# Performance work log

Measured on AMD Instinct MI355X. Metric: run time of the kernel, lower is better.

Reference implementation:

```python
import jax, jax.numpy as jnp
import numpy as np

DIM = 1024
QK_DIM = 128
HIDDEN = 2048  # int(2.0 * DIM)
B, N = 4, 4096


def setup_inputs() -> dict:
    key = jax.random.key(0)
    ks = jax.random.split(key, 10)
    std = 0.02
    return {
        "x": jax.random.normal(ks[0], (B, N, DIM), dtype=jnp.float32),
        "ln_g": jnp.ones((DIM,), jnp.float32),
        "ln_b": jnp.zeros((DIM,), jnp.float32),
        "W_hidden": jax.random.normal(ks[1], (DIM, 2 * HIDDEN), jnp.float32) * (1.0 / np.sqrt(DIM)),
        "b_hidden": jnp.zeros((2 * HIDDEN,), jnp.float32),
        "W_qk": jax.random.normal(ks[2], (DIM, QK_DIM), jnp.float32) * (1.0 / np.sqrt(DIM)),
        "b_qk": jnp.zeros((QK_DIM,), jnp.float32),
        "os_gamma": jax.random.normal(ks[3], (2, QK_DIM), jnp.float32) * std,
        "os_beta": jnp.zeros((2, QK_DIM), jnp.float32),
        "W_out": jax.random.normal(ks[4], (HIDDEN, DIM), jnp.float32) * (1.0 / np.sqrt(HIDDEN)),
        "b_out": jnp.zeros((DIM,), jnp.float32),
    }


def _layernorm(x, g, b, eps=1e-5):
    mu = jnp.mean(x, axis=-1, keepdims=True)
    var = jnp.var(x, axis=-1, keepdims=True)
    return (x - mu) * jax.lax.rsqrt(var + eps) * g + b


def reference(x, ln_g, ln_b, W_hidden, b_hidden, W_qk, b_qk, os_gamma, os_beta, W_out, b_out):
    n = x.shape[-2]
    normed = _layernorm(x, ln_g, ln_b)
    hidden = jax.nn.silu(normed @ W_hidden + b_hidden)  # [b,n,2*hidden]
    v, gate = jnp.split(hidden, 2, axis=-1)             # [b,n,hidden] each
    qk = jax.nn.silu(normed @ W_qk + b_qk)              # [b,n,qk]
    q = qk * os_gamma[0] + os_beta[0]
    k = qk * os_gamma[1] + os_beta[1]
    sim = jnp.einsum('bid,bjd->bij', q, k)
    # causal: divide row i by (i+1)
    denom = (jnp.arange(n, dtype=x.dtype) + 1.0)[:, None]  # [n,1]
    sim = sim / denom
    attn = jnp.square(jax.nn.relu(sim))
    causal_mask = jnp.triu(jnp.ones((n, n), dtype=bool), k=1)
    attn = jnp.where(causal_mask, 0.0, attn)
    out = jnp.einsum('bij,bjd->bid', attn, v)
    out = out * gate
    out = out @ W_out + b_out
    return out + x
```

## Files before the change

kernel.cpp:

```cpp
#include <hip/hip_runtime.h>
#include <hip/hip_bf16.h>
#include <stdint.h>

typedef __bf16 bf16_t;
typedef __bf16 bf16x4 __attribute__((ext_vector_type(4)));
typedef __bf16 bf16x8 __attribute__((ext_vector_type(8)));
typedef float  f32x4  __attribute__((ext_vector_type(4)));

#define MFMA16(a, b, c) __builtin_amdgcn_mfma_f32_16x16x32_bf16((a), (b), (c), 0, 0, 0)

static constexpr int TOKS   = 16384;
static constexpr int SEQ    = 4096;
static constexpr int DIMK   = 1024;
static constexpr int H2     = 4096;
static constexpr int HID    = 2048;
static constexpr int QKD    = 128;
static constexpr int SMEM8P = 131072;
static constexpr size_t PBATCH = 8912896;

__device__ __forceinline__ void gload_lds16(const bf16_t* g, bf16_t* l) {
  __builtin_amdgcn_global_load_lds((__attribute__((address_space(1))) void*)(g),
                                   (__attribute__((address_space(3))) void*)(l),
                                   16, 0, 0);
}

__device__ __forceinline__ float silu_f(float v) { return v / (1.0f + __expf(-v)); }

#define BARRIER() do { __builtin_amdgcn_sched_barrier(0); \
                       __builtin_amdgcn_s_barrier();      \
                       __builtin_amdgcn_sched_barrier(0); } while (0)

__global__ __launch_bounds__(256) void k_transpose_bf16(const float* __restrict__ W,
                                                        bf16_t* __restrict__ WT,
                                                        int K, int N) {
  __shared__ float t[32][33];
  int n0 = blockIdx.x * 32, k0 = blockIdx.y * 32;
  int tx = threadIdx.x & 31, ty = threadIdx.x >> 5;
#pragma unroll
  for (int r = 0; r < 32; r += 8)
    t[ty + r][tx] = W[(size_t)(k0 + ty + r) * N + n0 + tx];
  __syncthreads();
#pragma unroll
  for (int r = 0; r < 32; r += 8)
    WT[(size_t)(n0 + ty + r) * K + k0 + tx] = (bf16_t)t[tx][ty + r];
}

__global__ __launch_bounds__(256) void k_layernorm(const float* __restrict__ x,
                                                   const float* __restrict__ g,
                                                   const float* __restrict__ b,
                                                   bf16_t* __restrict__ out) {
  int row = blockIdx.x, t = threadIdx.x;
  const float4* xr = (const float4*)(x + (size_t)row * DIMK);
  float4 v = xr[t];
  float s  = v.x + v.y + v.z + v.w;
  float ss = v.x * v.x + v.y * v.y + v.z * v.z + v.w * v.w;
#pragma unroll
  for (int o = 1; o < 64; o <<= 1) { s += __shfl_xor(s, o); ss += __shfl_xor(ss, o); }
  __shared__ float red[8];
  int wave = t >> 6, lane = t & 63;
  if (lane == 0) { red[wave] = s; red[wave + 4] = ss; }
  __syncthreads();
  s  = red[0] + red[1] + red[2] + red[3];
  ss = red[4] + red[5] + red[6] + red[7];
  float mean = s * (1.0f / DIMK);
  float var  = ss * (1.0f / DIMK) - mean * mean;
  float rstd = rsqrtf(var + 1e-5f);
  float4 gg = ((const float4*)g)[t];
  float4 bb = ((const float4*)b)[t];
  bf16x4 o4;
  o4[0] = (bf16_t)((v.x - mean) * rstd * gg.x + bb.x);
  o4[1] = (bf16_t)((v.y - mean) * rstd * gg.y + bb.y);
  o4[2] = (bf16_t)((v.z - mean) * rstd * gg.z + bb.z);
  o4[3] = (bf16_t)((v.w - mean) * rstd * gg.w + bb.w);
  *(bf16x4*)(out + (size_t)row * DIMK + t * 4) = o4;
}

#define MFMAQ(MH, KK)                                                         \
  _Pragma("unroll")                                                           \
  for (int mi = 0; mi < 4; ++mi)                                              \
    _Pragma("unroll")                                                         \
    for (int nj = 0; nj < 4; ++nj)                                            \
      acc[(MH) * 4 + mi][nj] =                                                \
          MFMA16(aF[(MH) * 4 + mi][KK], bF[nj][KK], acc[(MH) * 4 + mi][nj]);

__device__ __forceinline__ void core8p(const bf16_t* __restrict__ Ag, int lda,
                                       const bf16_t* __restrict__ Bg, int ldb,
                                       int NK, bf16_t* AS, bf16_t* BS,
                                       f32x4 (&acc)[8][4]) {
  const int tid = threadIdx.x, wid = tid >> 6, lane = tid & 63;
  const int wm = wid >> 2, wn = wid & 3;
  const int srow = lane >> 3;
  const int scol = ((lane & 7) ^ srow) * 8;

  auto stA = [&](int kt, int h) {
    const bf16_t* s = Ag + (size_t)(h * 128 + wid * 16 + srow) * lda + kt * 64 + scol;
    bf16_t* d = AS + ((kt & 1) * 2 + h) * 8192 + wid * 1024;
    gload_lds16(s, d);
    gload_lds16(s + 8 * lda, d + 512);
  };
  auto stB = [&](int kt, int h) {
    const bf16_t* s = Bg + (size_t)(h * 128 + wid * 16 + srow) * ldb + kt * 64 + scol;
    bf16_t* d = BS + ((kt & 1) * 2 + h) * 8192 + wid * 1024;
    gload_lds16(s, d);
    gload_lds16(s + 8 * ldb, d + 512);
  };

  const int g0 = (lane >> 4) ^ (lane & 7);
  const bf16_t* pA0 = AS + wm * 8192 + (lane & 15) * 64 + g0 * 8;
  const bf16_t* pA1 = AS + wm * 8192 + (lane & 15) * 64 + (g0 ^ 4) * 8;
  const bf16_t* pB0 = BS + (wn >> 1) * 8192 + ((wn & 1) * 64 + (lane & 15)) * 64 + g0 * 8;
  const bf16_t* pB1 = BS + (wn >> 1) * 8192 + ((wn & 1) * 64 + (lane & 15)) * 64 + (g0 ^ 4) * 8;

  bf16x8 aF[8][2], bF[4][2];

  stA(0, 0); stA(0, 1); stB(0, 0); stB(0, 1);
  stA(1, 0); stA(1, 1);
  asm volatile("s_waitcnt vmcnt(4)" ::: "memory");
  BARRIER();

  for (int g = 0; g < NK; ++g) {
    const int buf = (g & 1) * 16384;
#pragma unroll
    for (int mi = 0; mi < 8; ++mi) aF[mi][0] = *(const bf16x8*)(pA0 + buf + mi * 1024);
#pragma unroll
    for (int nj = 0; nj < 4; ++nj) bF[nj][0] = *(const bf16x8*)(pB0 + buf + nj * 1024);
    if (g + 1 < NK) stB(g + 1, 0);
    BARRIER();
    __builtin_amdgcn_s_setprio(1);
    MFMAQ(0, 0);
    __builtin_amdgcn_s_setprio(0);
    BARRIER();
#pragma unroll
    for (int mi = 0; mi < 8; ++mi) aF[mi][1] = *(const bf16x8*)(pA1 + buf + mi * 1024);
    if (g + 1 < NK) stB(g + 1, 1);
    BARRIER();
    __builtin_amdgcn_s_setprio(1);
    MFMAQ(1, 0);
    __builtin_amdgcn_s_setprio(0);
    BARRIER();
#pragma unroll
    for (int nj = 0; nj < 4; ++nj) bF[nj][1] = *(const bf16x8*)(pB1 + buf + nj * 1024);
    if (g + 2 < NK) stA(g + 2, 0);
    BARRIER();
    __builtin_amdgcn_s_setprio(1);
    MFMAQ(0, 1);
    __builtin_amdgcn_s_setprio(0);
    BARRIER();
    if (g + 2 < NK) stA(g + 2, 1);
    BARRIER();
    __builtin_amdgcn_s_setprio(1);
    MFMAQ(1, 1);
    __builtin_amdgcn_s_setprio(0);
    if (g < NK - 2)       { asm volatile("s_waitcnt vmcnt(4)" ::: "memory"); }
    else if (g == NK - 2) { asm volatile("s_waitcnt vmcnt(0)" ::: "memory"); }
    BARRIER();
  }
}

__global__ __launch_bounds__(512, 2) void k_gemm_hidden8p(const bf16_t* __restrict__ A,
                                                          const bf16_t* __restrict__ BT,
                                                          const float* __restrict__ bias,
                                                          bf16_t* __restrict__ vT,
                                                          bf16_t* __restrict__ gate) {
  extern __shared__ __align__(16) char lds[];
  bf16_t* AS = (bf16_t*)lds;
  bf16_t* BS = AS + 32768;
  const int nwg = gridDim.x, bid = blockIdx.x;
  const int swz = (bid & 7) * (nwg >> 3) + (bid >> 3);
  const int mblk = swz >> 4, nblk = swz & 15;
  const int m0 = mblk * 256, n0 = nblk * 256;
  f32x4 acc[8][4];
#pragma unroll
  for (int i = 0; i < 8; ++i)
#pragma unroll
    for (int j = 0; j < 4; ++j) acc[i][j] = (f32x4){0.f, 0.f, 0.f, 0.f};
  core8p(A + (size_t)m0 * DIMK, DIMK, BT + (size_t)n0 * DIMK, DIMK,
         DIMK / 64, AS, BS, acc);

  const int tid = threadIdx.x, wid = tid >> 6, lane = tid & 63;
  const int wm = wid >> 2, wn = wid & 3;
  const int row0 = m0 + wm * 128, col0 = n0 + wn * 64;
#pragma unroll
  for (int mi = 0; mi < 8; ++mi)
#pragma unroll
    for (int nj = 0; nj < 4; ++nj) {
      int col = col0 + nj * 16 + (lane & 15);
      float bv = bias[col];
      int row = row0 + mi * 16 + ((lane >> 4) << 2);
      float sv[4];
#pragma unroll
      for (int r = 0; r < 4; ++r) sv[r] = silu_f(acc[mi][nj][r] + bv);
      if (col < HID) {
        bf16x4 pk;
#pragma unroll
        for (int r = 0; r < 4; ++r) pk[r] = (bf16_t)sv[r];
        *(bf16x4*)(vT + (size_t)col * TOKS + row) = pk;
      } else {
#pragma unroll
        for (int r = 0; r < 4; ++r)
          gate[(size_t)(row + r) * HID + (col - HID)] = (bf16_t)sv[r];
      }
    }
}

__global__ __launch_bounds__(512, 2) void k_gemm_out8p(const bf16_t* __restrict__ A,
                                                       const bf16_t* __restrict__ BT,
                                                       const float* __restrict__ bo,
                                                       const float* __restrict__ x,
                                                       float* __restrict__ out) {
  extern __shared__ __align__(16) char lds[];
  bf16_t* AS = (bf16_t*)lds;
  bf16_t* BS = AS + 32768;
  const int nwg = gridDim.x, bid = blockIdx.x;
  const int swz = (bid & 7) * (nwg >> 3) + (bid >> 3);
  const int mblk = swz >> 2, nblk = swz & 3;
  const int m0 = mblk * 256, n0 = nblk * 256;
  f32x4 acc[8][4];
#pragma unroll
  for (int i = 0; i < 8; ++i)
#pragma unroll
    for (int j = 0; j < 4; ++j) acc[i][j] = (f32x4){0.f, 0.f, 0.f, 0.f};
  core8p(A + (size_t)m0 * HID, HID, BT + (size_t)n0 * HID, HID,
         HID / 64, AS, BS, acc);

  const int tid = threadIdx.x, wid = tid >> 6, lane = tid & 63;
  const int wm = wid >> 2, wn = wid & 3;
  const int row0 = m0 + wm * 128, col0 = n0 + wn * 64;
#pragma unroll
  for (int mi = 0; mi < 8; ++mi)
#pragma unroll
    for (int nj = 0; nj < 4; ++nj) {
      int col = col0 + nj * 16 + (lane & 15);
      float bv = bo[col];
      int row = row0 + mi * 16 + ((lane >> 4) << 2);
#pragma unroll
      for (int r = 0; r < 4; ++r) {
        size_t gi = (size_t)(row + r) * DIMK + col;
        out[gi] = acc[mi][nj][r] + bv + x[gi];
      }
    }
}

__global__ __launch_bounds__(512, 2) void k_pv8p(const bf16_t* __restrict__ Pb,
                                                 const bf16_t* __restrict__ vT,
                                                 bf16_t* __restrict__ gate) {
  extern __shared__ __align__(16) char lds[];
  bf16_t* AS = (bf16_t*)lds;
  bf16_t* BS = AS + 32768;
  const int w = blockIdx.x;
  const int rb = 15 - (w >> 5);
  const int hb = (w >> 2) & 7;
  const int bb = w & 3;
  const int lda = (rb + 1) * 256;
  const bf16_t* Ag = Pb + (size_t)bb * PBATCH + (size_t)65536 * (rb * (rb + 1) / 2);
  const bf16_t* Bg = vT + (size_t)(hb * 256) * TOKS + (size_t)bb * SEQ;
  f32x4 acc[8][4];
#pragma unroll
  for (int i = 0; i < 8; ++i)
#pragma unroll
    for (int j = 0; j < 4; ++j) acc[i][j] = (f32x4){0.f, 0.f, 0.f, 0.f};
  core8p(Ag, lda, Bg, TOKS, (rb + 1) * 4, AS, BS, acc);

  const int tid = threadIdx.x, wid = tid >> 6, lane = tid & 63;
  const int wm = wid >> 2, wn = wid & 3;
  const int row0 = rb * 256 + wm * 128, col0 = hb * 256 + wn * 64;
#pragma unroll
  for (int mi = 0; mi < 8; ++mi)
#pragma unroll
    for (int nj = 0; nj < 4; ++nj) {
      int col = col0 + nj * 16 + (lane & 15);
      int row = row0 + mi * 16 + ((lane >> 4) << 2);
#pragma unroll
      for (int r = 0; r < 4; ++r) {
        size_t gi = (size_t)(bb * SEQ + row + r) * HID + col;
        float gv = (float)gate[gi];
        gate[gi] = (bf16_t)(acc[mi][nj][r] * gv);
      }
    }
}

__device__ __forceinline__ void gemm_core_std(const bf16_t* __restrict__ Ag0, int lda,
                                              const bf16_t* __restrict__ Bg0, int ldb,
                                              int K, bf16_t* As, bf16_t* Bs,
                                              f32x4 acc[4][4]) {
  const int tid = threadIdx.x;
  const int wave = tid >> 6, lane = tid & 63;
  bf16_t* asw = As + wave * 32 * 32;
  bf16_t* bsw = Bs + wave * 32 * 32;
  const int ar = ((wave >> 1) * 64 + (lane & 15)) * 32 + (lane >> 4) * 8;
  const int br = ((wave & 1) * 64 + (lane & 15)) * 32 + (lane >> 4) * 8;
  for (int k0 = 0; k0 < K; k0 += 32) {
    __syncthreads();
    gload_lds16(Ag0 + k0, asw);
    gload_lds16(Ag0 + k0 + 16 * lda, asw + 16 * 32);
    gload_lds16(Bg0 + k0, bsw);
    gload_lds16(Bg0 + k0 + 16 * ldb, bsw + 16 * 32);
    __syncthreads();
    bf16x8 af[4], bfr[4];
#pragma unroll
    for (int m = 0; m < 4; m++) af[m] = *(const bf16x8*)(As + ar + m * 16 * 32);
#pragma unroll
    for (int n = 0; n < 4; n++) bfr[n] = *(const bf16x8*)(Bs + br + n * 16 * 32);
#pragma unroll
    for (int m = 0; m < 4; m++)
#pragma unroll
      for (int n = 0; n < 4; n++) acc[m][n] = MFMA16(af[m], bfr[n], acc[m][n]);
  }
}

__global__ __launch_bounds__(256) void k_gemm_qk(const bf16_t* __restrict__ A,
                                                 const bf16_t* __restrict__ BT,
                                                 const float* __restrict__ bias,
                                                 const float* __restrict__ osg,
                                                 const float* __restrict__ osb,
                                                 bf16_t* __restrict__ qo,
                                                 bf16_t* __restrict__ ko) {
  __shared__ __align__(16) bf16_t As[128 * 32];
  __shared__ __align__(16) bf16_t Bs[128 * 32];
  const int tid = threadIdx.x, wave = tid >> 6, lane = tid & 63;
  const int m0 = blockIdx.y * 128;
  const bf16_t* Ag0 = A + (size_t)(m0 + wave * 32 + (lane >> 2)) * DIMK + (lane & 3) * 8;
  const bf16_t* Bg0 = BT + (size_t)(wave * 32 + (lane >> 2)) * DIMK + (lane & 3) * 8;
  f32x4 acc[4][4];
#pragma unroll
  for (int m = 0; m < 4; m++)
#pragma unroll
    for (int n = 0; n < 4; n++) acc[m][n] = (f32x4){0.f, 0.f, 0.f, 0.f};
  gemm_core_std(Ag0, DIMK, Bg0, DIMK, DIMK, As, Bs, acc);

  const int row0 = m0 + (wave >> 1) * 64;
  const int col0 = (wave & 1) * 64;
#pragma unroll
  for (int m = 0; m < 4; m++) {
#pragma unroll
    for (int n = 0; n < 4; n++) {
      int col = col0 + n * 16 + (lane & 15);
      float bv = bias[col];
      float g0 = osg[col], b0 = osb[col];
      float g1 = osg[QKD + col], b1 = osb[QKD + col];
      int row = row0 + m * 16 + ((lane >> 4) << 2);
#pragma unroll
      for (int r = 0; r < 4; r++) {
        float sv = silu_f(acc[m][n][r] + bv);
        qo[(size_t)(row + r) * QKD + col] = (bf16_t)(sv * g0 + b0);
        ko[(size_t)(row + r) * QKD + col] = (bf16_t)(sv * g1 + b1);
      }
    }
  }
}

__global__ __launch_bounds__(256) void k_qkt(const bf16_t* __restrict__ qb,
                                             const bf16_t* __restrict__ kb,
                                             bf16_t* __restrict__ Pb) {
  const int jb = blockIdx.x, ib = blockIdx.y, bb = blockIdx.z;
  const int rb = ib >> 1;
  if (jb > 2 * rb + 1) return;
  const int lda = (rb + 1) * 256;
  bf16_t* Pt = Pb + (size_t)bb * PBATCH + (size_t)65536 * (rb * (rb + 1) / 2)
             + (size_t)((ib & 1) * 128) * lda + jb * 128;
  if (jb == ib + 1) {
    const int row = threadIdx.x >> 1, cb = (threadIdx.x & 1) * 64;
    bf16x8 z;
#pragma unroll
    for (int i = 0; i < 8; ++i) z[i] = (bf16_t)0.0f;
#pragma unroll
    for (int c = 0; c < 64; c += 8)
      *(bf16x8*)(Pt + (size_t)row * lda + cb + c) = z;
    return;
  }
  __shared__ __align__(16) bf16_t As[128 * 32];
  __shared__ __align__(16) bf16_t Bs[128 * 32];
  const int tid = threadIdx.x, wave = tid >> 6, lane = tid & 63;
  const bf16_t* Ag0 = qb + (size_t)(bb * SEQ + ib * 128 + wave * 32 + (lane >> 2)) * QKD + (lane & 3) * 8;
  const bf16_t* Bg0 = kb + (size_t)(bb * SEQ + jb * 128 + wave * 32 + (lane >> 2)) * QKD + (lane & 3) * 8;
  f32x4 acc[4][4];
#pragma unroll
  for (int m = 0; m < 4; m++)
#pragma unroll
    for (int n = 0; n < 4; n++) acc[m][n] = (f32x4){0.f, 0.f, 0.f, 0.f};
  gemm_core_std(Ag0, QKD, Bg0, QKD, QKD, As, Bs, acc);

  const int il0 = (wave >> 1) * 64, jl0 = (wave & 1) * 64;
#pragma unroll
  for (int m = 0; m < 4; m++) {
#pragma unroll
    for (int n = 0; n < 4; n++) {
      int jloc = jl0 + n * 16 + (lane & 15);
      int jg = jb * 128 + jloc;
#pragma unroll
      for (int r = 0; r < 4; r++) {
        int iloc = il0 + m * 16 + ((lane >> 4) << 2) + r;
        int ig = ib * 128 + iloc;
        float sv = acc[m][n][r] / (float)(ig + 1);
        sv = fmaxf(sv, 0.f);
        sv *= sv;
        if (jg > ig) sv = 0.f;
        Pt[(size_t)iloc * lda + jloc] = (bf16_t)sv;
      }
    }
  }
}

extern "C" void kernel_launch(void* const* d_in, const int* in_sizes, int n_in,
                              void* d_out, int out_size, void* d_ws, size_t ws_size,
                              hipStream_t stream) {
  (void)in_sizes; (void)n_in; (void)out_size; (void)ws_size;
  const float* x    = (const float*)d_in[0];
  const float* ln_g = (const float*)d_in[1];
  const float* ln_b = (const float*)d_in[2];
  const float* Wh   = (const float*)d_in[3];
  const float* bh   = (const float*)d_in[4];
  const float* Wqk  = (const float*)d_in[5];
  const float* bqk  = (const float*)d_in[6];
  const float* osg  = (const float*)d_in[7];
  const float* osb  = (const float*)d_in[8];
  const float* Wo   = (const float*)d_in[9];
  const float* bo   = (const float*)d_in[10];
  float* out = (float*)d_out;

  char* ws = (char*)d_ws;
  bf16_t* normed = (bf16_t*)ws;  ws += (size_t)TOKS * DIMK * 2;
  bf16_t* WhT    = (bf16_t*)ws;  ws += (size_t)H2 * DIMK * 2;
  bf16_t* WqkT   = (bf16_t*)ws;  ws += (size_t)QKD * DIMK * 2;
  bf16_t* WoT    = (bf16_t*)ws;  ws += (size_t)DIMK * HID * 2;
  bf16_t* gate   = (bf16_t*)ws;  ws += (size_t)TOKS * HID * 2;
  bf16_t* vT     = (bf16_t*)ws;  ws += (size_t)HID * TOKS * 2;
  bf16_t* qb     = (bf16_t*)ws;  ws += (size_t)TOKS * QKD * 2;
  bf16_t* kb     = (bf16_t*)ws;  ws += (size_t)TOKS * QKD * 2;
  bf16_t* Pb     = (bf16_t*)ws;  ws += (size_t)4 * PBATCH * 2;

  hipFuncSetAttribute((const void*)k_gemm_hidden8p,
                      hipFuncAttributeMaxDynamicSharedMemorySize, SMEM8P);
  hipFuncSetAttribute((const void*)k_gemm_out8p,
                      hipFuncAttributeMaxDynamicSharedMemorySize, SMEM8P);
  hipFuncSetAttribute((const void*)k_pv8p,
                      hipFuncAttributeMaxDynamicSharedMemorySize, SMEM8P);

  k_transpose_bf16<<<dim3(H2 / 32, DIMK / 32), 256, 0, stream>>>(Wh, WhT, DIMK, H2);
  k_transpose_bf16<<<dim3(QKD / 32, DIMK / 32), 256, 0, stream>>>(Wqk, WqkT, DIMK, QKD);
  k_transpose_bf16<<<dim3(DIMK / 32, HID / 32), 256, 0, stream>>>(Wo, WoT, HID, DIMK);
  k_layernorm<<<TOKS, 256, 0, stream>>>(x, ln_g, ln_b, normed);
  k_gemm_hidden8p<<<dim3((TOKS / 256) * (H2 / 256)), 512, SMEM8P, stream>>>(normed, WhT, bh, vT, gate);
  k_gemm_qk<<<dim3(1, TOKS / 128), 256, 0, stream>>>(normed, WqkT, bqk, osg, osb, qb, kb);
  k_qkt<<<dim3(SEQ / 128, SEQ / 128, 4), 256, 0, stream>>>(qb, kb, Pb);
  k_pv8p<<<dim3(16 * 8 * 4), 512, SMEM8P, stream>>>(Pb, vT, gate);
  k_gemm_out8p<<<dim3((TOKS / 256) * (DIMK / 256)), 512, SMEM8P, stream>>>(gate, WoT, bo, x, out);
}
```

Before: 482.7 us.

## Restructure GEMM mainloop into unrolled two-stage pipeline with split fragment loads

```diff
diff --git a/kernel.cpp b/kernel.cpp
--- a/kernel.cpp
+++ b/kernel.cpp
@@ -83,6 +83,25 @@
       acc[(MH) * 4 + mi][nj] =                                                \
           MFMA16(aF[(MH) * 4 + mi][KK], bF[nj][KK], acc[(MH) * 4 + mi][nj]);
 
+#define RD_A0(BUFE)                                                           \
+  _Pragma("unroll")                                                           \
+  for (int mi = 0; mi < 4; ++mi) aF[mi][0] = *(const bf16x8*)(pA0 + (BUFE) + mi * 1024);
+#define RD_A0H(BUFE)                                                          \
+  _Pragma("unroll")                                                           \
+  for (int mi = 4; mi < 8; ++mi) aF[mi][0] = *(const bf16x8*)(pA0 + (BUFE) + mi * 1024);
+#define RD_A1L(BUFE)                                                          \
+  _Pragma("unroll")                                                           \
+  for (int mi = 0; mi < 4; ++mi) aF[mi][1] = *(const bf16x8*)(pA1 + (BUFE) + mi * 1024);
+#define RD_A1H(BUFE)                                                          \
+  _Pragma("unroll")                                                           \
+  for (int mi = 4; mi < 8; ++mi) aF[mi][1] = *(const bf16x8*)(pA1 + (BUFE) + mi * 1024);
+#define RD_B0(BUFE)                                                           \
+  _Pragma("unroll")                                                           \
+  for (int nj = 0; nj < 4; ++nj) bF[nj][0] = *(const bf16x8*)(pB0 + (BUFE) + nj * 1024);
+#define RD_B1(BUFE)                                                           \
+  _Pragma("unroll")                                                           \
+  for (int nj = 0; nj < 4; ++nj) bF[nj][1] = *(const bf16x8*)(pB1 + (BUFE) + nj * 1024);
+
 __device__ __forceinline__ void core8p(const bf16_t* __restrict__ Ag, int lda,
                                        const bf16_t* __restrict__ Bg, int ldb,
                                        int NK, bf16_t* AS, bf16_t* BS,
@@ -92,18 +111,23 @@
   const int srow = lane >> 3;
   const int scol = ((lane & 7) ^ srow) * 8;
 
-  auto stA = [&](int kt, int h) {
-    const bf16_t* s = Ag + (size_t)(h * 128 + wid * 16 + srow) * lda + kt * 64 + scol;
-    bf16_t* d = AS + ((kt & 1) * 2 + h) * 8192 + wid * 1024;
-    gload_lds16(s, d);
-    gload_lds16(s + 8 * lda, d + 512);
-  };
-  auto stB = [&](int kt, int h) {
-    const bf16_t* s = Bg + (size_t)(h * 128 + wid * 16 + srow) * ldb + kt * 64 + scol;
-    bf16_t* d = BS + ((kt & 1) * 2 + h) * 8192 + wid * 1024;
-    gload_lds16(s, d);
-    gload_lds16(s + 8 * ldb, d + 512);
-  };
+  const bf16_t* aS0a = Ag + (size_t)(wid * 16 + srow) * lda + scol;
+  const bf16_t* aS0b = aS0a + (size_t)8 * lda;
+  const bf16_t* aS1a = aS0a + (size_t)128 * lda;
+  const bf16_t* aS1b = aS1a + (size_t)8 * lda;
+  const bf16_t* bS0a = Bg + (size_t)(wid * 16 + srow) * ldb + scol;
+  const bf16_t* bS0b = bS0a + (size_t)8 * ldb;
+  const bf16_t* bS1a = bS0a + (size_t)128 * ldb;
+  const bf16_t* bS1b = bS1a + (size_t)8 * ldb;
+
+  bf16_t* const dA00 = AS + wid * 1024;
+  bf16_t* const dA01 = AS + 8192  + wid * 1024;
+  bf16_t* const dA10 = AS + 16384 + wid * 1024;
+  bf16_t* const dA11 = AS + 24576 + wid * 1024;
+  bf16_t* const dB00 = BS + wid * 1024;
+  bf16_t* const dB01 = BS + 8192  + wid * 1024;
+  bf16_t* const dB10 = BS + 16384 + wid * 1024;
+  bf16_t* const dB11 = BS + 24576 + wid * 1024;
 
   const int g0 = (lane >> 4) ^ (lane & 7);
   const bf16_t* pA0 = AS + wm * 8192 + (lane & 15) * 64 + g0 * 8;
@@ -113,47 +137,77 @@
 
   bf16x8 aF[8][2], bF[4][2];
 
-  stA(0, 0); stA(0, 1); stB(0, 0); stB(0, 1);
-  stA(1, 0); stA(1, 1);
+  gload_lds16(aS0a,      dA00); gload_lds16(aS0b,      dA00 + 512);
+  gload_lds16(aS1a,      dA01); gload_lds16(aS1b,      dA01 + 512);
+  gload_lds16(bS0a,      dB00); gload_lds16(bS0b,      dB00 + 512);
+  gload_lds16(bS1a,      dB01); gload_lds16(bS1b,      dB01 + 512);
+  gload_lds16(bS0a + 64, dB10); gload_lds16(bS0b + 64, dB10 + 512);
+  gload_lds16(bS1a + 64, dB11); gload_lds16(bS1b + 64, dB11 + 512);
   asm volatile("s_waitcnt vmcnt(4)" ::: "memory");
   BARRIER();
-
-  for (int g = 0; g < NK; ++g) {
-    const int buf = (g & 1) * 16384;
-#pragma unroll
-    for (int mi = 0; mi < 8; ++mi) aF[mi][0] = *(const bf16x8*)(pA0 + buf + mi * 1024);
-#pragma unroll
-    for (int nj = 0; nj < 4; ++nj) bF[nj][0] = *(const bf16x8*)(pB0 + buf + nj * 1024);
-    if (g + 1 < NK) stB(g + 1, 0);
-    BARRIER();
-    __builtin_amdgcn_s_setprio(1);
-    MFMAQ(0, 0);
-    __builtin_amdgcn_s_setprio(0);
-    BARRIER();
-#pragma unroll
-    for (int mi = 0; mi < 8; ++mi) aF[mi][1] = *(const bf16x8*)(pA1 + buf + mi * 1024);
-    if (g + 1 < NK) stB(g + 1, 1);
-    BARRIER();
-    __builtin_amdgcn_s_setprio(1);
-    MFMAQ(1, 0);
-    __builtin_amdgcn_s_setprio(0);
-    BARRIER();
-#pragma unroll
-    for (int nj = 0; nj < 4; ++nj) bF[nj][1] = *(const bf16x8*)(pB1 + buf + nj * 1024);
-    if (g + 2 < NK) stA(g + 2, 0);
-    BARRIER();
-    __builtin_amdgcn_s_setprio(1);
-    MFMAQ(0, 1);
-    __builtin_amdgcn_s_setprio(0);
-    BARRIER();
-    if (g + 2 < NK) stA(g + 2, 1);
-    BARRIER();
-    __builtin_amdgcn_s_setprio(1);
-    MFMAQ(1, 1);
-    __builtin_amdgcn_s_setprio(0);
-    if (g < NK - 2)       { asm volatile("s_waitcnt vmcnt(4)" ::: "memory"); }
-    else if (g == NK - 2) { asm volatile("s_waitcnt vmcnt(0)" ::: "memory"); }
-    BARRIER();
+  RD_A0(0);
+  RD_B0(0);
+
+  for (int g = 0; g < NK; g += 2) {
+    const bool more = (g + 2 < NK);
+    RD_A0H(0);
+    gload_lds16(aS0a + 64, dA10); gload_lds16(aS0b + 64, dA10 + 512);
+    BARRIER();
+    __builtin_amdgcn_s_setprio(1); MFMAQ(0, 0); __builtin_amdgcn_s_setprio(0);
+    BARRIER();
+    RD_A1L(0);
+    RD_B1(0);
+    gload_lds16(aS1a + 64, dA11); gload_lds16(aS1b + 64, dA11 + 512);
+    BARRIER();
+    __builtin_amdgcn_s_setprio(1); MFMAQ(1, 0); __builtin_amdgcn_s_setprio(0);
+    BARRIER();
+    RD_A1H(0);
+    BARRIER();
+    __builtin_amdgcn_s_setprio(1); MFMAQ(0, 1); __builtin_amdgcn_s_setprio(0);
+    BARRIER();
+    if (more) {
+      gload_lds16(bS0a + 128, dB00); gload_lds16(bS0b + 128, dB00 + 512);
+      gload_lds16(bS1a + 128, dB01); gload_lds16(bS1b + 128, dB01 + 512);
+      asm volatile("s_waitcnt vmcnt(4)" ::: "memory");
+    } else {
+      asm volatile("s_waitcnt vmcnt(0)" ::: "memory");
+    }
+    BARRIER();
+    RD_A0(16384);
+    RD_B0(16384);
+    __builtin_amdgcn_s_setprio(1); MFMAQ(1, 1); __builtin_amdgcn_s_setprio(0);
+    BARRIER();
+
+    RD_A0H(16384);
+    if (more) { gload_lds16(aS0a + 128, dA00); gload_lds16(aS0b + 128, dA00 + 512); }
+    BARRIER();
+    __builtin_amdgcn_s_setprio(1); MFMAQ(0, 0); __builtin_amdgcn_s_setprio(0);
+    BARRIER();
+    RD_A1L(16384);
+    RD_B1(16384);
+    if (more) { gload_lds16(aS1a + 128, dA01); gload_lds16(aS1b + 128, dA01 + 512); }
+    BARRIER();
+    __builtin_amdgcn_s_setprio(1); MFMAQ(1, 0); __builtin_amdgcn_s_setprio(0);
+    BARRIER();
+    RD_A1H(16384);
+    BARRIER();
+    __builtin_amdgcn_s_setprio(1); MFMAQ(0, 1); __builtin_amdgcn_s_setprio(0);
+    BARRIER();
+    if (more) {
+      gload_lds16(bS0a + 192, dB10); gload_lds16(bS0b + 192, dB10 + 512);
+      gload_lds16(bS1a + 192, dB11); gload_lds16(bS1b + 192, dB11 + 512);
+      asm volatile("s_waitcnt vmcnt(4)" ::: "memory");
+      BARRIER();
+      RD_A0(0);
+      RD_B0(0);
+    } else {
+      BARRIER();
+    }
+    __builtin_amdgcn_s_setprio(1); MFMAQ(1, 1); __builtin_amdgcn_s_setprio(0);
+    BARRIER();
+
+    aS0a += 128; aS0b += 128; aS1a += 128; aS1b += 128;
+    bS0a += 128; bS0b += 128; bS1a += 128; bS1b += 128;
   }
 }
 
```

New measurement: 922.8 us. +91.2%, slower.
